# Kernel optimization log

Hardware: AMD Instinct MI355X
Metric: run time of the kernel (lower is better)

Reference implementation:

```python
import jax, jax.numpy as jnp
import numpy as np

B, N, C = 4, 8192, 512
H = 4
D = C // H  # 128
HID = 4 * C  # mlp hidden, mlp_ratio=4.0
SCALE = D ** -0.5
EPS = 1e-5


def layernorm(x, w, b):
    mu = jnp.mean(x, axis=-1, keepdims=True)
    var = jnp.var(x, axis=-1, keepdims=True)
    return (x - mu) * jax.lax.rsqrt(var + EPS) * w + b


def setup_inputs() -> dict:
    key = jax.random.key(0)
    ks = jax.random.split(key, 8)
    s = lambda fan_in: 1.0 / np.sqrt(fan_in)
    return {
        "x": jax.random.normal(ks[0], (B, N, C), jnp.float32),
        "norm1_w": jnp.ones((C,), jnp.float32),
        "norm1_b": jnp.zeros((C,), jnp.float32),
        "qkv_w": jax.random.normal(ks[1], (C, 3 * C), jnp.float32) * s(C),
        "qkv_b": jnp.zeros((3 * C,), jnp.float32),
        "lnk_w": jnp.ones((D,), jnp.float32),
        "lnk_b": jnp.zeros((D,), jnp.float32),
        "lnv_w": jnp.ones((D,), jnp.float32),
        "lnv_b": jnp.zeros((D,), jnp.float32),
        "proj_w": jax.random.normal(ks[2], (C, C), jnp.float32) * s(C),
        "proj_b": jnp.zeros((C,), jnp.float32),
        "norm2_w": jnp.ones((C,), jnp.float32),
        "norm2_b": jnp.zeros((C,), jnp.float32),
        "mlp_w1": jax.random.normal(ks[3], (C, HID), jnp.float32) * s(C),
        "mlp_b1": jnp.zeros((HID,), jnp.float32),
        "mlp_w2": jax.random.normal(ks[4], (HID, C), jnp.float32) * s(HID),
        "mlp_b2": jnp.zeros((C,), jnp.float32),
    }


def reference(x, norm1_w, norm1_b, qkv_w, qkv_b, lnk_w, lnk_b, lnv_w, lnv_b,
              proj_w, proj_b, norm2_w, norm2_b, mlp_w1, mlp_b1, mlp_w2, mlp_b2):
    shortcut = x
    xn = layernorm(x, norm1_w, norm1_b)
    qkv = xn @ qkv_w + qkv_b                       # [B,N,3C]
    qkv = qkv.reshape(B, N, 3, H, D).transpose(2, 0, 3, 1, 4)  # [3,B,H,N,D]
    q, k, v = qkv[0], qkv[1], qkv[2]
    k = layernorm(k, lnk_w, lnk_b)
    v = layernorm(v, lnv_w, lnv_b)
    context = jnp.einsum('bhnd,bhne->bhde', k, v)   # [B,H,D,D] small context
    attn = jnp.einsum('bhnd,bhde->bhne', q, context) * SCALE  # [B,H,N,D]
    attn = attn.transpose(0, 2, 1, 3).reshape(B, N, C)
    x1 = shortcut + (attn @ proj_w + proj_b)
    h = layernorm(x1, norm2_w, norm2_b)
    mlp = jax.nn.gelu(h @ mlp_w1 + mlp_b1, approximate=False) @ mlp_w2 + mlp_b2
    return x1 + mlp
```

## Files before the change

### kernel.cpp

```cpp
#include <hip/hip_runtime.h>
#include <stdint.h>


#define B_    4
#define N_    8192
#define C_    512
#define H_    4
#define D_    128
#define HID_  2048
#define M_    (B_*N_)
#define EPS_  1e-5f
#define SCALE_ 0.08838834764831845f

typedef unsigned short u16;
typedef unsigned int u32;
typedef __attribute__((ext_vector_type(8))) __bf16 bfrag_t;
typedef __attribute__((ext_vector_type(4))) float  f4_t;
typedef __attribute__((ext_vector_type(2))) u32    u32x2;

__device__ __forceinline__ float bf2f(u16 a) {
    u32 u = ((u32)a) << 16; float f;
    __builtin_memcpy(&f, &u, 4); return f;
}
__device__ __forceinline__ u16 f2bf(float f) {
    u32 u; __builtin_memcpy(&u, &f, 4);
    u += 0x7FFFu + ((u >> 16) & 1u);
    return (u16)(u >> 16);
}
__device__ __forceinline__ u16 f2bf_fast(float f) {
    u32 u; __builtin_memcpy(&u, &f, 4);
    return (u16)((u + 0x8000u) >> 16);
}

__device__ __forceinline__ float fast_gelu(float x) {
    const float kA = 2.3022084f;
    const float kB = 0.1029435f;
    float x2 = x * x;
    float e1 = __builtin_amdgcn_exp2f(x * (kB * x2 + kA));
    return x - x * __builtin_amdgcn_rcpf(e1 + 1.0f);
}

__device__ __forceinline__ void gld16(u16* lds, const u16* g) {
    void* gp = const_cast<u16*>(g);
    __builtin_amdgcn_global_load_lds((__attribute__((address_space(1))) void*)gp,
                                     (__attribute__((address_space(3))) void*)lds,
                                     16, 0, 0);
}

__global__ __launch_bounds__(256)
void wtrans(const float* __restrict__ in, u16* __restrict__ out,
            int K, int Ncols) {
    const int nb = Ncols >> 6;
    const int k0 = (blockIdx.x / nb) << 6, n0 = (blockIdx.x % nb) << 6;
    __shared__ u16 tile[64][65];
    const int tx = threadIdx.x & 63, ty = threadIdx.x >> 6;
    #pragma unroll
    for (int r = 0; r < 16; ++r) {
        int k = ty + r * 4;
        tile[k][tx] = f2bf(in[(long)(k0 + k) * Ncols + n0 + tx]);
    }
    __syncthreads();
    #pragma unroll
    for (int r = 0; r < 16; ++r) {
        int n = ty + r * 4;
        out[(long)(n0 + n) * K + k0 + tx] = tile[tx][n];
    }
}

__global__ __launch_bounds__(256)
void ln_rows(const float* __restrict__ in, const float* __restrict__ w,
             const float* __restrict__ b, u16* __restrict__ out) {
    long row = blockIdx.x;
    int t = threadIdx.x;
    const float* p = in + row * 512;
    float v0 = p[t], v1 = p[t + 256];
    float s = v0 + v1, q = v0 * v0 + v1 * v1;
    #pragma unroll
    for (int o = 32; o >= 1; o >>= 1) { s += __shfl_xor(s, o, 64); q += __shfl_xor(q, o, 64); }
    __shared__ float sh[8];
    int wv = t >> 6, l = t & 63;
    if (l == 0) { sh[wv] = s; sh[4 + wv] = q; }
    __syncthreads();
    s = sh[0] + sh[1] + sh[2] + sh[3];
    q = sh[4] + sh[5] + sh[6] + sh[7];
    float mu = s * (1.f / 512.f);
    float var = q * (1.f / 512.f) - mu * mu;
    float rs = rsqrtf(var + EPS_);
    out[row * 512 + t]       = f2bf((v0 - mu) * rs * w[t] + b[t]);
    out[row * 512 + t + 256] = f2bf((v1 - mu) * rs * w[t + 256] + b[t + 256]);
}

__global__ __launch_bounds__(256)
void lnkv(const u16* __restrict__ qkv,
          const float* __restrict__ kw, const float* __restrict__ kb,
          const float* __restrict__ vw, const float* __restrict__ vb,
          u16* __restrict__ kT, u16* __restrict__ vT) {
    int bh = blockIdx.x;
    int b = bh >> 2, h = bh & 3;
    int n0 = blockIdx.y * 64;
    int wv = threadIdx.x >> 6, l = threadIdx.x & 63;
    __shared__ u16 lk[128 * 68], lv[128 * 68];

    for (int r = wv; r < 64; r += 4) {
        long base = ((long)b * N_ + n0 + r) * 1536 + h * 128;
        {
            float x0 = bf2f(qkv[base + 512 + l]), x1 = bf2f(qkv[base + 512 + 64 + l]);
            float s = x0 + x1, q = x0 * x0 + x1 * x1;
            #pragma unroll
            for (int o = 32; o >= 1; o >>= 1) { s += __shfl_xor(s, o, 64); q += __shfl_xor(q, o, 64); }
            float mu = s * (1.f / 128.f), var = q * (1.f / 128.f) - mu * mu;
            float rs = rsqrtf(var + EPS_);
            lk[l * 68 + r]        = f2bf((x0 - mu) * rs * kw[l] + kb[l]);
            lk[(l + 64) * 68 + r] = f2bf((x1 - mu) * rs * kw[l + 64] + kb[l + 64]);
        }
        {
            float x0 = bf2f(qkv[base + 1024 + l]), x1 = bf2f(qkv[base + 1024 + 64 + l]);
            float s = x0 + x1, q = x0 * x0 + x1 * x1;
            #pragma unroll
            for (int o = 32; o >= 1; o >>= 1) { s += __shfl_xor(s, o, 64); q += __shfl_xor(q, o, 64); }
            float mu = s * (1.f / 128.f), var = q * (1.f / 128.f) - mu * mu;
            float rs = rsqrtf(var + EPS_);
            lv[l * 68 + r]        = f2bf((x0 - mu) * rs * vw[l] + vb[l]);
            lv[(l + 64) * 68 + r] = f2bf((x1 - mu) * rs * vw[l + 64] + vb[l + 64]);
        }
    }
    __syncthreads();
    long obase = (long)bh * D_ * N_;
    #pragma unroll 4
    for (int i = 0; i < 32; i++) {
        int idx = i * 256 + threadIdx.x;
        int d = idx >> 6, nn = idx & 63;
        kT[obase + (long)d * N_ + n0 + nn] = lk[d * 68 + nn];
        vT[obase + (long)d * N_ + n0 + nn] = lv[d * 68 + nn];
    }
}

__global__ void ctxfin(const float* __restrict__ ctxP, u16* __restrict__ ctxN) {
    int idx = blockIdx.x * 256 + threadIdx.x;
    if (idx >= 16 * 16384) return;
    int bh = idx >> 14, r = idx & 16383;
    const float* p = ctxP + (long)bh * 262144 + r;
    float s = 0.f;
    #pragma unroll
    for (int q = 0; q < 16; q++) s += p[q * 16384];
    ctxN[idx] = f2bf(s * SCALE_);
}

template<int MODE, int KTOT, int ZDIV>
__global__ __launch_bounds__(256)
void gemm_bt(const u16* __restrict__ A, int lda, int64_t aZ1, int64_t aZ2,
             const u16* __restrict__ Bt, int ldb, int64_t bZ1, int64_t bZ2,
             void* __restrict__ outv, int ldo, int64_t oZ1, int64_t oZ2,
             const float* __restrict__ bias, const float* __restrict__ resid, int ldr) {
    __shared__ __align__(16) u16 sA[128 * 32];
    __shared__ __align__(16) u16 sB[128 * 32];
    const int z = blockIdx.z;
    const int z1 = z / ZDIV, z2 = z % ZDIV;
    A  += z1 * aZ1 + z2 * aZ2;
    Bt += z1 * bZ1 + z2 * bZ2;
    const int64_t ooff = z1 * oZ1 + z2 * oZ2;
    const int m0 = blockIdx.x * 128, n0 = blockIdx.y * 128;
    const int tid = threadIdx.x, wave = tid >> 6, lane = tid & 63;
    const int wr = wave >> 1, wc = wave & 1;

    f4_t acc[4][4];
    #pragma unroll
    for (int i = 0; i < 4; i++)
        #pragma unroll
        for (int j = 0; j < 4; j++) acc[i][j] = (f4_t){0.f, 0.f, 0.f, 0.f};

    const int c0 = wave * 64 + lane, c1 = 256 + wave * 64 + lane;
    const int r0 = c0 >> 2, e0 = (c0 & 3) * 8;
    const int r1 = c1 >> 2, e1 = (c1 & 3) * 8;
    const u16* a0 = A + (int64_t)(m0 + r0) * lda + e0;
    const u16* a1 = A + (int64_t)(m0 + r1) * lda + e1;
    const u16* b0 = Bt + (int64_t)(n0 + r0) * ldb + e0;
    const u16* b1 = Bt + (int64_t)(n0 + r1) * ldb + e1;
    u16* lA0 = &sA[wave * 512];        u16* lA1 = &sA[2048 + wave * 512];
    u16* lB0 = &sB[wave * 512];        u16* lB1 = &sB[2048 + wave * 512];

    const int qd = lane >> 4, md = lane & 15;
    int aoff[4], boff[4];
    #pragma unroll
    for (int i = 0; i < 4; i++) {
        aoff[i] = (wr * 64 + i * 16 + md) * 32 + qd * 8;
        boff[i] = (wc * 64 + i * 16 + md) * 32 + qd * 8;
    }

    #pragma unroll 4
    for (int kt = 0; kt < KTOT; kt += 32) {
        __syncthreads();
        gld16(lA0, a0 + kt);  gld16(lA1, a1 + kt);
        gld16(lB0, b0 + kt);  gld16(lB1, b1 + kt);
        __syncthreads();
        bfrag_t af[4], bf[4];
        #pragma unroll
        for (int i = 0; i < 4; i++) af[i] = *(const bfrag_t*)&sA[aoff[i]];
        #pragma unroll
        for (int i = 0; i < 4; i++) bf[i] = *(const bfrag_t*)&sB[boff[i]];
        #pragma unroll
        for (int mi = 0; mi < 4; mi++)
            #pragma unroll
            for (int ni = 0; ni < 4; ni++)
                acc[mi][ni] = __builtin_amdgcn_mfma_f32_16x16x32_bf16(
                    af[mi], bf[ni], acc[mi][ni], 0, 0, 0);
    }

    #pragma unroll
    for (int mi = 0; mi < 4; mi++) {
        #pragma unroll
        for (int r = 0; r < 4; r++) {
            int m = m0 + wr * 64 + mi * 16 + qd * 4 + r;
            int64_t rowo = ooff + (int64_t)m * ldo;
            #pragma unroll
            for (int ni = 0; ni < 4; ni++) {
                int n = n0 + wc * 64 + ni * 16 + md;
                float v = acc[mi][ni][r];
                if (MODE == 0)
                    ((u16*)outv)[rowo + n] = f2bf_fast(v);
                else
                    ((float*)outv)[rowo + n] = v;
            }
        }
    }
}

#define LD_(p)      (*(const bfrag_t*)(p))
#define FENCE_      asm volatile("" ::: "memory")
#define BAR_        do { FENCE_; __builtin_amdgcn_s_barrier(); FENCE_; } while (0)
#define WVM4_       asm volatile("s_waitcnt vmcnt(4)" ::: "memory")
#define WVM0_       asm volatile("s_waitcnt vmcnt(0)" ::: "memory")
#define MFMA_(va, vb, c) c = __builtin_amdgcn_mfma_f32_16x16x32_bf16(va, vb, c, 0, 0, 0)
#define MM16_(I0) do { __builtin_amdgcn_s_setprio(1); \
  MFMA_(b0,a0,acc[(I0)+0][0]); MFMA_(b1,a0,acc[(I0)+0][1]); MFMA_(b2,a0,acc[(I0)+0][2]); MFMA_(b3,a0,acc[(I0)+0][3]); \
  MFMA_(b0,a1,acc[(I0)+1][0]); MFMA_(b1,a1,acc[(I0)+1][1]); MFMA_(b2,a1,acc[(I0)+1][2]); MFMA_(b3,a1,acc[(I0)+1][3]); \
  MFMA_(b0,a2,acc[(I0)+2][0]); MFMA_(b1,a2,acc[(I0)+2][1]); MFMA_(b2,a2,acc[(I0)+2][2]); MFMA_(b3,a2,acc[(I0)+2][3]); \
  MFMA_(b0,a3,acc[(I0)+3][0]); MFMA_(b1,a3,acc[(I0)+3][1]); MFMA_(b2,a3,acc[(I0)+3][2]); MFMA_(b3,a3,acc[(I0)+3][3]); \
  __builtin_amdgcn_s_setprio(0); } while (0)
#define STGA_(nb, kk, tt) do { \
  u16* d_ = lds + (nb) * 32768 + (kk) * 8192 + wid * 512; \
  const u16* s_ = aS + (int64_t)(tt) * 64 + (kk) * 32; \
  gld16(d_, s_); gld16(d_ + 4096, s_ + a128); } while (0)
#define STGB_(nb, kk, tt) do { \
  u16* d_ = lds + (nb) * 32768 + 16384 + (kk) * 8192 + wid * 512; \
  const u16* s_ = bS + (int64_t)(tt) * 64 + (kk) * 32; \
  gld16(d_, s_); gld16(d_ + 4096, s_ + b128); } while (0)

template<int MODE, int KTOT>
__global__ __launch_bounds__(512, 2)
void gemm256(const u16* __restrict__ A, int lda, int64_t aZ,
             const u16* __restrict__ Bt, int ldb, int64_t bZ,
             void* __restrict__ outv, int ldo, int64_t oZ,
             const float* __restrict__ bias, const float* __restrict__ resid, int ldr) {
    __shared__ __align__(16) u16 lds[65536];
    const int z = blockIdx.z;
    A += (int64_t)z * aZ;
    Bt += (int64_t)z * bZ;
    const int64_t ooff = (int64_t)z * oZ;
    const int gx = gridDim.x, gy = gridDim.y;
    const int lid = blockIdx.x + blockIdx.y * gx;
    int bx, by;
    if ((gx & 7) == 0) {
        const int j = lid >> 3;
        bx = (gx >> 3) * (lid & 7) + j / gy;
        by = j % gy;
    } else { bx = blockIdx.x; by = blockIdx.y; }
    const int m0 = bx * 256, n0 = by * 256;
    const int tid = threadIdx.x, wid = tid >> 6, lane = tid & 63;
    const int wr = wid >> 2, wc = wid & 3;
    const int md = lane & 15, qd = lane >> 4;

    f4_t acc[8][4];
    #pragma unroll
    for (int i = 0; i < 8; ++i)
        #pragma unroll
        for (int j = 0; j < 4; ++j) acc[i][j] = (f4_t){0.f, 0.f, 0.f, 0.f};

    const int srow = tid >> 2;
    const int scol = ((tid & 3) ^ ((tid >> 3) & 3)) * 8;
    const u16* aS = A  + (int64_t)(m0 + srow) * lda + scol;
    const u16* bS = Bt + (int64_t)(n0 + srow) * ldb + scol;
    const int64_t a128 = (int64_t)lda * 128, b128 = (int64_t)ldb * 128;

    const int xq = (qd ^ ((md >> 1) & 3)) * 16;
    const int aRow = (wr * 128 + md) * 64;
    const int bRow = (wc * 64 + md) * 64;
    const char* ldsc = (const char*)lds;

    constexpr int NT = KTOT / 64;

    {
        STGA_(0, 0, 0); STGB_(0, 0, 0); STGA_(0, 1, 0); STGB_(0, 1, 0);
        WVM4_; BAR_;
    }

    #pragma unroll 2
    for (int t = 0; t < NT; ++t) {
        const int cur = t & 1, nb = cur ^ 1;
        const char* cA = ldsc + cur * 65536 + aRow;
        const char* cB = ldsc + cur * 65536 + 32768 + bRow;
        const bool st = (t + 1 < NT);
        bfrag_t a0, a1, a2, a3, b0, b1, b2, b3;

        a0 = LD_(cA + xq);        a1 = LD_(cA + 1024 + xq);
        a2 = LD_(cA + 2048 + xq); a3 = LD_(cA + 3072 + xq);
        b0 = LD_(cB + xq);        b1 = LD_(cB + 1024 + xq);
        b2 = LD_(cB + 2048 + xq); b3 = LD_(cB + 3072 + xq);
        if (st) STGA_(nb, 0, t + 1);
        BAR_;
        MM16_(0);

        a0 = LD_(cA + 4096 + xq); a1 = LD_(cA + 5120 + xq);
        a2 = LD_(cA + 6144 + xq); a3 = LD_(cA + 7168 + xq);
        if (st) STGB_(nb, 0, t + 1);
        BAR_;
        MM16_(4);

        if (st) { WVM4_; } else { WVM0_; }
        BAR_;

        a0 = LD_(cA + 16384 + xq);        a1 = LD_(cA + 17408 + xq);
        a2 = LD_(cA + 18432 + xq);        a3 = LD_(cA + 19456 + xq);
        b0 = LD_(cB + 16384 + xq);        b1 = LD_(cB + 17408 + xq);
        b2 = LD_(cB + 18432 + xq);        b3 = LD_(cB + 19456 + xq);
        if (st) STGA_(nb, 1, t + 1);
        BAR_;
        MM16_(0);

        a0 = LD_(cA + 20480 + xq); a1 = LD_(cA + 21504 + xq);
        a2 = LD_(cA + 22528 + xq); a3 = LD_(cA + 23552 + xq);
        if (st) STGB_(nb, 1, t + 1);
        BAR_;
        MM16_(4);

        if (st) { WVM4_; } else { WVM0_; }
        BAR_;
    }

    #pragma unroll
    for (int i = 0; i < 8; ++i) {
        const int m = m0 + wr * 128 + i * 16 + md;
        const int64_t rowo = ooff + (int64_t)m * ldo;
        #pragma unroll
        for (int j = 0; j < 4; ++j) {
            const int n = n0 + wc * 64 + j * 16 + qd * 4;
            f4_t v = acc[i][j];
            if (MODE == 1 || MODE == 2 || MODE == 3) {
                const f4_t bq = *(const f4_t*)&bias[n];
                v.x += bq.x; v.y += bq.y; v.z += bq.z; v.w += bq.w;
            }
            if (MODE == 2) {
                v.x = fast_gelu(v.x); v.y = fast_gelu(v.y);
                v.z = fast_gelu(v.z); v.w = fast_gelu(v.w);
            }
            if (MODE == 3) {
                const f4_t r4 = *(const f4_t*)&resid[ooff + (int64_t)m * ldr + n];
                v.x += r4.x; v.y += r4.y; v.z += r4.z; v.w += r4.w;
                *(f4_t*)&((float*)outv)[rowo + n] = v;
            } else {
                u32x2 pk;
                pk.x = (u32)f2bf_fast(v.x) | ((u32)f2bf_fast(v.y) << 16);
                pk.y = (u32)f2bf_fast(v.z) | ((u32)f2bf_fast(v.w) << 16);
                *(u32x2*)&((u16*)outv)[rowo + n] = pk;
            }
        }
    }
}

#undef LD_
#undef FENCE_
#undef BAR_
#undef WVM4_
#undef WVM0_
#undef MFMA_
#undef MM16_
#undef STGA_
#undef STGB_

extern "C" void kernel_launch(void* const* d_in, const int* in_sizes, int n_in,
                              void* d_out, int out_size, void* d_ws, size_t ws_size,
                              hipStream_t stream) {
    const float* x      = (const float*)d_in[0];
    const float* n1w    = (const float*)d_in[1];
    const float* n1b    = (const float*)d_in[2];
    const float* qkv_w  = (const float*)d_in[3];
    const float* qkv_b  = (const float*)d_in[4];
    const float* lnk_w  = (const float*)d_in[5];
    const float* lnk_b  = (const float*)d_in[6];
    const float* lnv_w  = (const float*)d_in[7];
    const float* lnv_b  = (const float*)d_in[8];
    const float* proj_w = (const float*)d_in[9];
    const float* proj_b = (const float*)d_in[10];
    const float* n2w    = (const float*)d_in[11];
    const float* n2b    = (const float*)d_in[12];
    const float* w1     = (const float*)d_in[13];
    const float* b1     = (const float*)d_in[14];
    const float* w2     = (const float*)d_in[15];
    const float* b2     = (const float*)d_in[16];
    float* out = (float*)d_out;

    char* ws = (char*)d_ws;
    u16*  qkvWT = (u16*)(ws + 0);
    u16*  projT = (u16*)(ws + 1572864);
    u16*  w1T   = (u16*)(ws + 2097152);
    u16*  w2T   = (u16*)(ws + 4194304);
    u16*  ctxN  = (u16*)(ws + 7340032);
    u16*  bufA  = (u16*)(ws + 7864320);
    u16*  qkv   = (u16*)(ws + 41418752);
    u16*  hid   = (u16*)(ws + 41418752);
    u16*  kT    = (u16*)(ws + 142082048);
    u16*  vT    = (u16*)(ws + 175636480);
    float* ctxP = (float*)(ws + 7864320);
    u16*  wqT   = (u16*)(ws + 7864320 + 16777216);

    dim3 blk(256);
    dim3 blk5(512);

    wtrans<<<dim3((512 / 64) * (1536 / 64)), blk, 0, stream>>>(qkv_w, qkvWT, 512, 1536);
    wtrans<<<dim3((512 / 64) * (512 / 64)),  blk, 0, stream>>>(proj_w, projT, 512, 512);
    wtrans<<<dim3((512 / 64) * (2048 / 64)), blk, 0, stream>>>(w1, w1T, 512, 2048);
    wtrans<<<dim3((2048 / 64) * (512 / 64)), blk, 0, stream>>>(w2, w2T, 2048, 512);

    ln_rows<<<dim3(M_), blk, 0, stream>>>(x, n1w, n1b, bufA);

    gemm256<1, 512><<<dim3(M_ / 256, 1536 / 256, 1), blk5, 0, stream>>>(
        bufA, 512, 0, qkvWT, 512, 0, (void*)qkv, 1536, 0, qkv_b, nullptr, 0);

    lnkv<<<dim3(B_ * H_, N_ / 64), blk, 0, stream>>>(qkv, lnk_w, lnk_b, lnv_w, lnv_b, kT, vT);

    gemm_bt<5, 512, 16><<<dim3(1, 1, B_ * H_ * 16), blk, 0, stream>>>(
        kT, N_, (int64_t)D_ * N_, 512,  vT, N_, (int64_t)D_ * N_, 512,
        (void*)ctxP, 128, 262144, 16384,  nullptr, nullptr, 0);
    ctxfin<<<dim3(16 * 16384 / 256), blk, 0, stream>>>(ctxP, ctxN);

    gemm_bt<0, 128, 4><<<dim3(4, 1, 16), blk, 0, stream>>>(
        projT, 512, 0, 128,  ctxN, 128, 65536, 16384,
        (void*)wqT, 512, 262144, 128,  nullptr, nullptr, 0);

    gemm256<3, 512><<<dim3(N_ / 256, 512 / 256, B_), blk5, 0, stream>>>(
        qkv, 1536, (int64_t)N_ * 1536,  wqT, 512, 262144,
        (void*)out, 512, (int64_t)N_ * 512,  proj_b, x, 512);

    ln_rows<<<dim3(M_), blk, 0, stream>>>(out, n2w, n2b, bufA);

    gemm256<2, 512><<<dim3(M_ / 256, HID_ / 256, 1), blk5, 0, stream>>>(
        bufA, 512, 0, w1T, 512, 0, (void*)hid, HID_, 0, b1, nullptr, 0);

    gemm256<3, 2048><<<dim3(M_ / 256, 512 / 256, 1), blk5, 0, stream>>>(
        hid, HID_, 0, w2T, HID_, 0, (void*)out, 512, 0, b2, out, 512);
}
```

Before: 549.7 us.

## Fuse K/V layernorm with context GEMM and change non-residual GEMM epilogue layout

```diff
diff --git a/kernel.cpp b/kernel.cpp
--- a/kernel.cpp
+++ b/kernel.cpp
@@ -91,58 +91,80 @@
 }
 
 __global__ __launch_bounds__(256)
-void lnkv(const u16* __restrict__ qkv,
-          const float* __restrict__ kw, const float* __restrict__ kb,
-          const float* __restrict__ vw, const float* __restrict__ vb,
-          u16* __restrict__ kT, u16* __restrict__ vT) {
-    int bh = blockIdx.x;
-    int b = bh >> 2, h = bh & 3;
-    int n0 = blockIdx.y * 64;
-    int wv = threadIdx.x >> 6, l = threadIdx.x & 63;
-    __shared__ u16 lk[128 * 68], lv[128 * 68];
-
-    for (int r = wv; r < 64; r += 4) {
-        long base = ((long)b * N_ + n0 + r) * 1536 + h * 128;
-        {
-            float x0 = bf2f(qkv[base + 512 + l]), x1 = bf2f(qkv[base + 512 + 64 + l]);
-            float s = x0 + x1, q = x0 * x0 + x1 * x1;
-            #pragma unroll
-            for (int o = 32; o >= 1; o >>= 1) { s += __shfl_xor(s, o, 64); q += __shfl_xor(q, o, 64); }
-            float mu = s * (1.f / 128.f), var = q * (1.f / 128.f) - mu * mu;
-            float rs = rsqrtf(var + EPS_);
-            lk[l * 68 + r]        = f2bf((x0 - mu) * rs * kw[l] + kb[l]);
-            lk[(l + 64) * 68 + r] = f2bf((x1 - mu) * rs * kw[l + 64] + kb[l + 64]);
-        }
-        {
-            float x0 = bf2f(qkv[base + 1024 + l]), x1 = bf2f(qkv[base + 1024 + 64 + l]);
-            float s = x0 + x1, q = x0 * x0 + x1 * x1;
-            #pragma unroll
-            for (int o = 32; o >= 1; o >>= 1) { s += __shfl_xor(s, o, 64); q += __shfl_xor(q, o, 64); }
-            float mu = s * (1.f / 128.f), var = q * (1.f / 128.f) - mu * mu;
-            float rs = rsqrtf(var + EPS_);
-            lv[l * 68 + r]        = f2bf((x0 - mu) * rs * vw[l] + vb[l]);
-            lv[(l + 64) * 68 + r] = f2bf((x1 - mu) * rs * vw[l + 64] + vb[l + 64]);
-        }
-    }
-    __syncthreads();
-    long obase = (long)bh * D_ * N_;
-    #pragma unroll 4
-    for (int i = 0; i < 32; i++) {
-        int idx = i * 256 + threadIdx.x;
-        int d = idx >> 6, nn = idx & 63;
-        kT[obase + (long)d * N_ + n0 + nn] = lk[d * 68 + nn];
-        vT[obase + (long)d * N_ + n0 + nn] = lv[d * 68 + nn];
-    }
+void lnkv_ctx(const u16* __restrict__ qkv,
+              const float* __restrict__ kw, const float* __restrict__ kb,
+              const float* __restrict__ vw, const float* __restrict__ vb,
+              float* __restrict__ ctxP) {
+    const int bh = blockIdx.x, b = bh >> 2, h = bh & 3;
+    const int nc = blockIdx.y;
+    const int wv = threadIdx.x >> 6, l = threadIdx.x & 63;
+    const int md = l & 15, qd = l >> 4;
+    __shared__ __align__(16) u16 lk[128 * 72], lv[128 * 72];
+
+    f4_t acc[8][2];
+    #pragma unroll
+    for (int i = 0; i < 8; ++i) { acc[i][0] = (f4_t){0,0,0,0}; acc[i][1] = (f4_t){0,0,0,0}; }
+
+    for (int ss = 0; ss < 4; ++ss) {
+        const int n0 = nc * 256 + ss * 64;
+        for (int r = wv; r < 64; r += 4) {
+            long base = ((long)b * N_ + n0 + r) * 1536 + h * 128;
+            {
+                float x0 = bf2f(qkv[base + 512 + l]), x1 = bf2f(qkv[base + 512 + 64 + l]);
+                float s = x0 + x1, q = x0 * x0 + x1 * x1;
+                #pragma unroll
+                for (int o = 32; o >= 1; o >>= 1) { s += __shfl_xor(s, o, 64); q += __shfl_xor(q, o, 64); }
+                float mu = s * (1.f / 128.f), var = q * (1.f / 128.f) - mu * mu;
+                float rs = rsqrtf(var + EPS_);
+                lk[l * 72 + r]        = f2bf((x0 - mu) * rs * kw[l] + kb[l]);
+                lk[(l + 64) * 72 + r] = f2bf((x1 - mu) * rs * kw[l + 64] + kb[l + 64]);
+            }
+            {
+                float x0 = bf2f(qkv[base + 1024 + l]), x1 = bf2f(qkv[base + 1024 + 64 + l]);
+                float s = x0 + x1, q = x0 * x0 + x1 * x1;
+                #pragma unroll
+                for (int o = 32; o >= 1; o >>= 1) { s += __shfl_xor(s, o, 64); q += __shfl_xor(q, o, 64); }
+                float mu = s * (1.f / 128.f), var = q * (1.f / 128.f) - mu * mu;
+                float rs = rsqrtf(var + EPS_);
+                lv[l * 72 + r]        = f2bf((x0 - mu) * rs * vw[l] + vb[l]);
+                lv[(l + 64) * 72 + r] = f2bf((x1 - mu) * rs * vw[l + 64] + vb[l + 64]);
+            }
+        }
+        __syncthreads();
+        #pragma unroll
+        for (int ks = 0; ks < 2; ++ks) {
+            const int ko = ks * 32 + qd * 8;
+            bfrag_t bf0 = *(const bfrag_t*)&lv[(wv * 32 + md) * 72 + ko];
+            bfrag_t bf1 = *(const bfrag_t*)&lv[(wv * 32 + 16 + md) * 72 + ko];
+            #pragma unroll
+            for (int db = 0; db < 8; ++db) {
+                bfrag_t af = *(const bfrag_t*)&lk[(db * 16 + md) * 72 + ko];
+                acc[db][0] = __builtin_amdgcn_mfma_f32_16x16x32_bf16(af, bf0, acc[db][0], 0, 0, 0);
+                acc[db][1] = __builtin_amdgcn_mfma_f32_16x16x32_bf16(af, bf1, acc[db][1], 0, 0, 0);
+            }
+        }
+        __syncthreads();
+    }
+    float* o = ctxP + ((long)bh * 32 + nc) * 16384;
+    #pragma unroll
+    for (int db = 0; db < 8; ++db)
+        #pragma unroll
+        for (int rr = 0; rr < 4; ++rr) {
+            const int d = db * 16 + qd * 4 + rr;
+            #pragma unroll
+            for (int eb = 0; eb < 2; ++eb)
+                o[d * 128 + wv * 32 + eb * 16 + md] = acc[db][eb][rr];
+        }
 }
 
 __global__ void ctxfin(const float* __restrict__ ctxP, u16* __restrict__ ctxN) {
     int idx = blockIdx.x * 256 + threadIdx.x;
     if (idx >= 16 * 16384) return;
     int bh = idx >> 14, r = idx & 16383;
-    const float* p = ctxP + (long)bh * 262144 + r;
+    const float* p = ctxP + (long)bh * 524288 + r;
     float s = 0.f;
     #pragma unroll
-    for (int q = 0; q < 16; q++) s += p[q * 16384];
+    for (int q = 0; q < 32; q++) s += p[q * 16384];
     ctxN[idx] = f2bf(s * SCALE_);
 }
 
@@ -231,12 +253,19 @@
 #define WVM4_       asm volatile("s_waitcnt vmcnt(4)" ::: "memory")
 #define WVM0_       asm volatile("s_waitcnt vmcnt(0)" ::: "memory")
 #define MFMA_(va, vb, c) c = __builtin_amdgcn_mfma_f32_16x16x32_bf16(va, vb, c, 0, 0, 0)
-#define MM16_(I0) do { __builtin_amdgcn_s_setprio(1); \
+#define MM16U_(I0) do { __builtin_amdgcn_s_setprio(1); \
+  MFMA_(a0,b0,acc[(I0)+0][0]); MFMA_(a0,b1,acc[(I0)+0][1]); MFMA_(a0,b2,acc[(I0)+0][2]); MFMA_(a0,b3,acc[(I0)+0][3]); \
+  MFMA_(a1,b0,acc[(I0)+1][0]); MFMA_(a1,b1,acc[(I0)+1][1]); MFMA_(a1,b2,acc[(I0)+1][2]); MFMA_(a1,b3,acc[(I0)+1][3]); \
+  MFMA_(a2,b0,acc[(I0)+2][0]); MFMA_(a2,b1,acc[(I0)+2][1]); MFMA_(a2,b2,acc[(I0)+2][2]); MFMA_(a2,b3,acc[(I0)+2][3]); \
+  MFMA_(a3,b0,acc[(I0)+3][0]); MFMA_(a3,b1,acc[(I0)+3][1]); MFMA_(a3,b2,acc[(I0)+3][2]); MFMA_(a3,b3,acc[(I0)+3][3]); \
+  __builtin_amdgcn_s_setprio(0); } while (0)
+#define MM16S_(I0) do { __builtin_amdgcn_s_setprio(1); \
   MFMA_(b0,a0,acc[(I0)+0][0]); MFMA_(b1,a0,acc[(I0)+0][1]); MFMA_(b2,a0,acc[(I0)+0][2]); MFMA_(b3,a0,acc[(I0)+0][3]); \
   MFMA_(b0,a1,acc[(I0)+1][0]); MFMA_(b1,a1,acc[(I0)+1][1]); MFMA_(b2,a1,acc[(I0)+1][2]); MFMA_(b3,a1,acc[(I0)+1][3]); \
   MFMA_(b0,a2,acc[(I0)+2][0]); MFMA_(b1,a2,acc[(I0)+2][1]); MFMA_(b2,a2,acc[(I0)+2][2]); MFMA_(b3,a2,acc[(I0)+2][3]); \
   MFMA_(b0,a3,acc[(I0)+3][0]); MFMA_(b1,a3,acc[(I0)+3][1]); MFMA_(b2,a3,acc[(I0)+3][2]); MFMA_(b3,a3,acc[(I0)+3][3]); \
   __builtin_amdgcn_s_setprio(0); } while (0)
+#define MM16_(I0) do { if (MODE == 3) MM16S_(I0); else MM16U_(I0); } while (0)
 #define STGA_(nb, kk, tt) do { \
   u16* d_ = lds + (nb) * 32768 + (kk) * 8192 + wid * 512; \
   const u16* s_ = aS + (int64_t)(tt) * 64 + (kk) * 32; \
@@ -337,31 +366,37 @@
         BAR_;
     }
 
-    #pragma unroll
-    for (int i = 0; i < 8; ++i) {
-        const int m = m0 + wr * 128 + i * 16 + md;
-        const int64_t rowo = ooff + (int64_t)m * ldo;
-        #pragma unroll
-        for (int j = 0; j < 4; ++j) {
-            const int n = n0 + wc * 64 + j * 16 + qd * 4;
-            f4_t v = acc[i][j];
-            if (MODE == 1 || MODE == 2 || MODE == 3) {
+    if (MODE == 3) {
+        #pragma unroll
+        for (int i = 0; i < 8; ++i) {
+            const int m = m0 + wr * 128 + i * 16 + md;
+            const int64_t rowo = ooff + (int64_t)m * ldo;
+            #pragma unroll
+            for (int j = 0; j < 4; ++j) {
+                const int n = n0 + wc * 64 + j * 16 + qd * 4;
+                f4_t v = acc[i][j];
                 const f4_t bq = *(const f4_t*)&bias[n];
                 v.x += bq.x; v.y += bq.y; v.z += bq.z; v.w += bq.w;
-            }
-            if (MODE == 2) {
-                v.x = fast_gelu(v.x); v.y = fast_gelu(v.y);
-                v.z = fast_gelu(v.z); v.w = fast_gelu(v.w);
-            }
-            if (MODE == 3) {
                 const f4_t r4 = *(const f4_t*)&resid[ooff + (int64_t)m * ldr + n];
                 v.x += r4.x; v.y += r4.y; v.z += r4.z; v.w += r4.w;
                 *(f4_t*)&((float*)outv)[rowo + n] = v;
-            } else {
-                u32x2 pk;
-                pk.x = (u32)f2bf_fast(v.x) | ((u32)f2bf_fast(v.y) << 16);
-                pk.y = (u32)f2bf_fast(v.z) | ((u32)f2bf_fast(v.w) << 16);
-                *(u32x2*)&((u16*)outv)[rowo + n] = pk;
+            }
+        }
+    } else {
+        #pragma unroll
+        for (int i = 0; i < 8; ++i) {
+            #pragma unroll
+            for (int rr = 0; rr < 4; ++rr) {
+                const int m = m0 + wr * 128 + i * 16 + qd * 4 + rr;
+                const int64_t rowo = ooff + (int64_t)m * ldo;
+                #pragma unroll
+                for (int j = 0; j < 4; ++j) {
+                    const int n = n0 + wc * 64 + j * 16 + md;
+                    float v = acc[i][j][rr];
+                    v += bias[n];
+                    if (MODE == 2) v = fast_gelu(v);
+                    ((u16*)outv)[rowo + n] = f2bf_fast(v);
+                }
             }
         }
     }
@@ -373,6 +408,8 @@
 #undef WVM4_
 #undef WVM0_
 #undef MFMA_
+#undef MM16U_
+#undef MM16S_
 #undef MM16_
 #undef STGA_
 #undef STGB_
@@ -408,10 +445,8 @@
     u16*  bufA  = (u16*)(ws + 7864320);
     u16*  qkv   = (u16*)(ws + 41418752);
     u16*  hid   = (u16*)(ws + 41418752);
-    u16*  kT    = (u16*)(ws + 142082048);
-    u16*  vT    = (u16*)(ws + 175636480);
+    u16*  wqT   = (u16*)(ws + 142082048);
     float* ctxP = (float*)(ws + 7864320);
-    u16*  wqT   = (u16*)(ws + 7864320 + 16777216);
 
     dim3 blk(256);
     dim3 blk5(512);
@@ -426,11 +461,8 @@
     gemm256<1, 512><<<dim3(M_ / 256, 1536 / 256, 1), blk5, 0, stream>>>(
         bufA, 512, 0, qkvWT, 512, 0, (void*)qkv, 1536, 0, qkv_b, nullptr, 0);
 
-    lnkv<<<dim3(B_ * H_, N_ / 64), blk, 0, stream>>>(qkv, lnk_w, lnk_b, lnv_w, lnv_b, kT, vT);
-
-    gemm_bt<5, 512, 16><<<dim3(1, 1, B_ * H_ * 16), blk, 0, stream>>>(
-        kT, N_, (int64_t)D_ * N_, 512,  vT, N_, (int64_t)D_ * N_, 512,
-        (void*)ctxP, 128, 262144, 16384,  nullptr, nullptr, 0);
+    lnkv_ctx<<<dim3(B_ * H_, 32), blk, 0, stream>>>(
+        qkv, lnk_w, lnk_b, lnv_w, lnv_b, ctxP);
     ctxfin<<<dim3(16 * 16384 / 256), blk, 0, stream>>>(ctxP, ctxN);
 
     gemm_bt<0, 128, 4><<<dim3(4, 1, 16), blk, 0, stream>>>(
```

New measurement: 549.8 us. About the same (+0.0%).
